# Performance work log

Hardware: AMD Instinct MI355X
Metric: run time of the kernel (lower is better)

The kernel has to match this reference:

```python
import jax, jax.numpy as jnp
import numpy as np

N_SRC0, N_DST0, FAN0 = 768000, 51200, 15
N_DST1, FAN1 = 5120, 10
N_DST2, FAN2 = 1024, 5
D_IN, D_HID, N_CLS = 128, 256, 47


def setup_inputs() -> dict:
    key = jax.random.key(0)
    ks = jax.random.split(key, 14)
    feats = jax.random.normal(ks[0], (N_SRC0, D_IN), jnp.float32)
    idx0 = jax.random.randint(ks[1], (N_DST0, FAN0), 0, N_SRC0)
    idx1 = jax.random.randint(ks[2], (N_DST1, FAN1), 0, N_DST0)
    idx2 = jax.random.randint(ks[3], (N_DST2, FAN2), 0, N_DST1)
    inverse_idx = jax.random.permutation(ks[4], N_DST0)
    s0 = 1.0 / np.sqrt(D_IN)
    s1 = 1.0 / np.sqrt(D_HID)
    return {
        "feats": feats,
        "W_self0": jax.random.normal(ks[5], (D_IN, D_HID), jnp.float32) * s0,
        "W_neigh0": jax.random.normal(ks[6], (D_IN, D_HID), jnp.float32) * s0,
        "b0": jnp.zeros((D_HID,), jnp.float32),
        "W_self1": jax.random.normal(ks[7], (D_HID, D_HID), jnp.float32) * s1,
        "W_neigh1": jax.random.normal(ks[8], (D_HID, D_HID), jnp.float32) * s1,
        "b1": jnp.zeros((D_HID,), jnp.float32),
        "W_self2": jax.random.normal(ks[9], (D_HID, N_CLS), jnp.float32) * s1,
        "W_neigh2": jax.random.normal(ks[10], (D_HID, N_CLS), jnp.float32) * s1,
        "b2": jnp.zeros((N_CLS,), jnp.float32),
        "idx0": idx0,
        "idx1": idx1,
        "idx2": idx2,
        "inverse_idx": inverse_idx,
    }


def _sage_mean(h, idx, W_self, W_neigh, b):
    # DGL SAGEConv('mean'): out = h_dst @ W_self + mean_neighbors(h) @ W_neigh + b
    h_dst = h[: idx.shape[0]]              # dst nodes are the first src nodes
    h_nb = jnp.take(h, idx, axis=0)        # [n_dst, fan, d] neighbor gather
    h_nb = h_nb.mean(axis=1)               # mean aggregation
    return h_dst @ W_self + h_nb @ W_neigh + b


def reference(feats, W_self0, W_neigh0, b0, W_self1, W_neigh1, b1,
              W_self2, W_neigh2, b2, idx0, idx1, idx2, inverse_idx):
    h = _sage_mean(feats, idx0, W_self0, W_neigh0, b0)
    h = h[inverse_idx]                     # NPFeatureShuffle inverse permutation
    h = jax.nn.relu(h)                     # dropout p=0 (eval)
    h = _sage_mean(h, idx1, W_self1, W_neigh1, b1)
    h = jax.nn.relu(h)
    h = _sage_mean(h, idx2, W_self2, W_neigh2, b2)
    return h
```

## Files before the change

kernel.cpp:

```cpp
#include <hip/hip_runtime.h>
#include <hip/hip_bf16.h>

#define N_SRC0 768000
#define N_DST0 51200
#define FAN0 15
#define N_DST1 5120
#define FAN1 10
#define N_DST2 1024
#define FAN2 5
#define D_IN 128
#define D_HID 256
#define N_CLS 47

#define TILES0 3200
#define GRID0 512

typedef __attribute__((ext_vector_type(4))) float f32x4;
typedef __attribute__((ext_vector_type(8))) short bf16x8;

static __device__ __forceinline__ unsigned pack_bf16(float x, float y) {
    __hip_bfloat16 hx = __float2bfloat16(x);
    __hip_bfloat16 hy = __float2bfloat16(y);
    unsigned short ux = *(unsigned short*)&hx;
    unsigned short uy = *(unsigned short*)&hy;
    return (unsigned)ux | ((unsigned)uy << 16);
}

__global__ void prep_weights(const float* __restrict__ Ws0, const float* __restrict__ Wn0,
                             const float* __restrict__ Ws1, const float* __restrict__ Wn1,
                             const float* __restrict__ Ws2, const float* __restrict__ Wn2,
                             float* __restrict__ Wc2,
                             __hip_bfloat16* __restrict__ Wt0b,
                             __hip_bfloat16* __restrict__ Wt1b)
{
    int t = blockIdx.x * blockDim.x + threadIdx.x;
    const int n2 = D_HID * N_CLS;
    if (t < n2) { Wc2[t] = Ws2[t]; Wc2[n2 + t] = Wn2[t]; }
    if (t < 65536) {
        int n = t >> 8, k = t & 255;
        float v = (k < 128) ? Ws0[k * 256 + n] : Wn0[(k - 128) * 256 + n];
        Wt0b[t] = __float2bfloat16(v);
    }
    if (t < 131072) {
        int n = t >> 9, k = t & 511;
        float v = (k < 256) ? Ws1[k * 256 + n] : Wn1[(k - 256) * 256 + n];
        Wt1b[t] = __float2bfloat16(v);
    }
}

__global__ __launch_bounds__(256, 2) void sage0_persist(
    const float* __restrict__ feats, const int* __restrict__ idx0,
    const int* __restrict__ inv, const __hip_bfloat16* __restrict__ Wt,
    const float* __restrict__ bias, unsigned short* __restrict__ H1b)
{
    __shared__ __align__(16) char xs[2][16 * 512];
    __shared__ int sidx[2][256];

    int tid = threadIdx.x;
    int bid = blockIdx.x;
    int w = tid >> 6, l = tid & 63;
    int lq = l & 15, kq = l >> 4;
    int rh = l >> 5, q = l & 31;

    bf16x8 B[4][8];
#pragma unroll
    for (int nt = 0; nt < 4; ++nt)
#pragma unroll
        for (int ks = 0; ks < 8; ++ks)
            B[nt][ks] = *(const bf16x8*)(Wt +
                (size_t)(w * 64 + nt * 16 + lq) * 256 + ks * 32 + kq * 8);
    float bv[4];
#pragma unroll
    for (int nt = 0; nt < 4; ++nt) bv[nt] = bias[w * 64 + nt * 16 + lq];

    int nIter = (TILES0 - bid + GRID0 - 1) / GRID0;

    {
        int r = tid >> 4, j = tid & 15;
        int rv = inv[bid * 16 + r];
        sidx[0][tid] = (j < 15) ? idx0[(size_t)rv * 15 + j] : rv;
    }
    __syncthreads();

    int pb = 0;
    for (int i = -1; i < nIter; ++i) {
        int t_cur = bid + i * GRID0;
        int t_nxt = t_cur + GRID0;
        bool mv = (i >= 0);
        bool gvv = (t_nxt < TILES0);
        int xb = pb ^ 1;
        const int* sp = sidx[pb];

        f32x4 acc[4];
#pragma unroll
        for (int nt = 0; nt < 4; ++nt) acc[nt] = (f32x4){0.f, 0.f, 0.f, 0.f};

        f32x4 s0 = (f32x4){0.f, 0.f, 0.f, 0.f};
#pragma unroll
        for (int ph = 0; ph < 4; ++ph) {
            int h = ph >> 1, jh = ph & 1;
            int r = w * 4 + h * 2 + rh;
            f32x4 g[8];
            if (gvv) {
                const int* sj = sp + r * 16 + jh * 8;
#pragma unroll
                for (int jj = 0; jj < 8; ++jj)
                    g[jj] = *(const f32x4*)&feats[(size_t)sj[jj] * 128 + q * 4];
            }
            if (mv) {
#pragma unroll
                for (int kss = 0; kss < 2; ++kss) {
                    int ks = ph * 2 + kss;
                    bf16x8 af = *(bf16x8*)(xs[pb] +
                        ((lq * 512 + ks * 64 + kq * 16) ^ ((lq & 7) << 4)));
#pragma unroll
                    for (int nt = 0; nt < 4; ++nt)
                        acc[nt] = __builtin_amdgcn_mfma_f32_16x16x32_bf16(
                            af, B[nt][ks], acc[nt], 0, 0, 0);
                }
            }
            if (gvv) {
                if (jh == 0) {
                    s0 = ((g[0] + g[1]) + (g[2] + g[3])) + ((g[4] + g[5]) + (g[6] + g[7]));
                } else {
                    f32x4 m = s0 + ((g[0] + g[1]) + (g[2] + g[3])) + ((g[4] + g[5]) + g[6]);
                    m *= (1.0f / 15.0f);
                    f32x4 sv = g[7];
                    uint2 ps = {pack_bf16(sv.x, sv.y), pack_bf16(sv.z, sv.w)};
                    uint2 pm = {pack_bf16(m.x, m.y), pack_bf16(m.z, m.w)};
                    int xorv = (r & 7) << 4;
                    *(uint2*)(xs[xb] + ((r * 512 + q * 8) ^ xorv)) = ps;
                    *(uint2*)(xs[xb] + ((r * 512 + 256 + q * 8) ^ xorv)) = pm;
                }
            }
        }

        if (mv) {
#pragma unroll
            for (int nt = 0; nt < 4; ++nt) {
#pragma unroll
                for (int qd = 0; qd < 4; ++qd) {
                    int row = t_cur * 16 + kq * 4 + qd;
                    float v = fmaxf(acc[nt][qd] + bv[nt], 0.f);
                    __hip_bfloat16 hb = __float2bfloat16(v);
                    H1b[(size_t)row * 256 + w * 64 + nt * 16 + lq] =
                        *(unsigned short*)&hb;
                }
            }
        }

        int t_n2 = t_nxt + GRID0;
        if (t_n2 < TILES0) {
            int r = tid >> 4, j = tid & 15;
            int rv = inv[t_n2 * 16 + r];
            sidx[xb][tid] = (j < 15) ? idx0[(size_t)rv * 15 + j] : rv;
        }
        __syncthreads();
        pb ^= 1;
    }
}

__global__ __launch_bounds__(512) void sage1_fused(
    const unsigned short* __restrict__ H1b, const int* __restrict__ idx1,
    const __hip_bfloat16* __restrict__ Wt,
    const float* __restrict__ bias, float* __restrict__ H2)
{
    __shared__ __align__(16) char xs[16 * 1024];
    __shared__ int sidx[16 * 12];

    int tid = threadIdx.x;
    int i0 = blockIdx.x * 16;

    for (int p = tid; p < 16 * 10; p += 512) {
        int r = p / 10, j = p % 10;
        sidx[r * 12 + j] = idx1[(size_t)(i0 + r) * 10 + j];
    }
    __syncthreads();

    int w = tid >> 6;
    int l = tid & 63;
    int rh = l >> 5, q = l & 31;

    {
        int r = w * 2 + rh;
        const int* sj = sidx + r * 12;
        uint4 sv = *(const uint4*)&H1b[(size_t)(i0 + r) * 256 + q * 8];
        f32x4 a0 = (f32x4){0.f, 0.f, 0.f, 0.f};
        f32x4 a1 = (f32x4){0.f, 0.f, 0.f, 0.f};
#pragma unroll
        for (int j = 0; j < 10; ++j) {
            uint4 nv = *(const uint4*)&H1b[(size_t)sj[j] * 256 + q * 8];
            a0.x += __uint_as_float(nv.x << 16);
            a0.y += __uint_as_float(nv.x & 0xffff0000u);
            a0.z += __uint_as_float(nv.y << 16);
            a0.w += __uint_as_float(nv.y & 0xffff0000u);
            a1.x += __uint_as_float(nv.z << 16);
            a1.y += __uint_as_float(nv.z & 0xffff0000u);
            a1.z += __uint_as_float(nv.w << 16);
            a1.w += __uint_as_float(nv.w & 0xffff0000u);
        }
        a0 *= (1.0f / 10.0f);
        a1 *= (1.0f / 10.0f);
        uint4 pm;
        pm.x = pack_bf16(a0.x, a0.y);
        pm.y = pack_bf16(a0.z, a0.w);
        pm.z = pack_bf16(a1.x, a1.y);
        pm.w = pack_bf16(a1.z, a1.w);
        int xorv = (r & 7) << 4;
        *(uint4*)(xs + ((r * 1024 + q * 16) ^ xorv)) = sv;
        *(uint4*)(xs + ((r * 1024 + 512 + q * 16) ^ xorv)) = pm;
    }
    __syncthreads();

    int arow = l & 15;
    int kq = l >> 4;
    int xorv_a = (arow & 7) << 4;

    f32x4 acc[2];
    acc[0] = (f32x4){0.f, 0.f, 0.f, 0.f};
    acc[1] = (f32x4){0.f, 0.f, 0.f, 0.f};

#pragma unroll
    for (int ks = 0; ks < 16; ++ks) {
        bf16x8 afrag = *(bf16x8*)(xs + ((arow * 1024 + ks * 64 + kq * 16) ^ xorv_a));
#pragma unroll
        for (int nt = 0; nt < 2; ++nt) {
            int n = w * 32 + nt * 16 + (l & 15);
            bf16x8 bfrag = *(const bf16x8*)(Wt + (size_t)n * 512 + ks * 32 + kq * 8);
            acc[nt] = __builtin_amdgcn_mfma_f32_16x16x32_bf16(afrag, bfrag, acc[nt], 0, 0, 0);
        }
    }

    int col0 = l & 15;
    int rq = l >> 4;
#pragma unroll
    for (int nt = 0; nt < 2; ++nt) {
        int col = w * 32 + nt * 16 + col0;
        float bvv = bias[col];
#pragma unroll
        for (int qd = 0; qd < 4; ++qd) {
            int row = i0 + rq * 4 + qd;
            H2[(size_t)row * 256 + col] = fmaxf(acc[nt][qd] + bvv, 0.f);
        }
    }
}

__global__ __launch_bounds__(256) void layer2(const float* __restrict__ H2,
                                              const int* __restrict__ idx2,
                                              const float* __restrict__ Wc2,
                                              const float* __restrict__ b2,
                                              float* __restrict__ out)
{
    __shared__ float xsf[512];
    __shared__ float part[4][64];
    int d = blockIdx.x;
    int t = threadIdx.x;
    const int* id = idx2 + (size_t)d * FAN2;

    xsf[t] = H2[(size_t)d * 256 + t];
    float a = 0.f;
#pragma unroll
    for (int j = 0; j < FAN2; ++j)
        a += H2[(size_t)id[j] * 256 + t];
    xsf[256 + t] = a * (1.0f / FAN2);
    __syncthreads();

    int c = t & 63;
    int kq = t >> 6;
    float s = 0.f;
    if (c < N_CLS) {
        int kbase = kq * 128;
#pragma unroll 8
        for (int k = 0; k < 128; ++k)
            s = fmaf(xsf[kbase + k], Wc2[(size_t)(kbase + k) * N_CLS + c], s);
    }
    part[kq][c] = s;
    __syncthreads();
    if (t < N_CLS) {
        float v = part[0][t] + part[1][t] + part[2][t] + part[3][t] + b2[t];
        out[(size_t)d * N_CLS + t] = v;
    }
}

extern "C" void kernel_launch(void* const* d_in, const int* in_sizes, int n_in,
                              void* d_out, int out_size, void* d_ws, size_t ws_size,
                              hipStream_t stream)
{
    const float* feats = (const float*)d_in[0];
    const float* Ws0 = (const float*)d_in[1];
    const float* Wn0 = (const float*)d_in[2];
    const float* b0  = (const float*)d_in[3];
    const float* Ws1 = (const float*)d_in[4];
    const float* Wn1 = (const float*)d_in[5];
    const float* b1  = (const float*)d_in[6];
    const float* Ws2 = (const float*)d_in[7];
    const float* Wn2 = (const float*)d_in[8];
    const float* b2  = (const float*)d_in[9];
    const int* idx0 = (const int*)d_in[10];
    const int* idx1 = (const int*)d_in[11];
    const int* idx2 = (const int*)d_in[12];
    const int* inv  = (const int*)d_in[13];

    char* ws = (char*)d_ws;
    unsigned short* H1b = (unsigned short*)ws;
    float* H2  = (float*)(ws + (size_t)N_DST0 * 256 * 2);
    float* Wc2 = H2 + (size_t)N_DST1 * 256;
    __hip_bfloat16* Wt0b = (__hip_bfloat16*)(Wc2 + 2 * D_HID * N_CLS);
    __hip_bfloat16* Wt1b = Wt0b + 256 * 256;

    prep_weights<<<dim3(512), dim3(256), 0, stream>>>(Ws0, Wn0, Ws1, Wn1, Ws2, Wn2,
                                                      Wc2, Wt0b, Wt1b);
    sage0_persist<<<dim3(GRID0), dim3(256), 0, stream>>>(feats, idx0, inv, Wt0b,
                                                         b0, H1b);
    sage1_fused<<<dim3(N_DST1 / 16), dim3(512), 0, stream>>>(H1b, idx1, Wt1b, b1, H2);
    layer2<<<dim3(N_DST2), dim3(256), 0, stream>>>(H2, idx2, Wc2, b2, (float*)d_out);
}
```

Measured before the change: 110.3 us.

## Fold weight prep into layer kernels and process two rows per layer2 block

Removes the separate prep_weights launch. sage0_persist now converts W0 to bf16 directly from the fp32 source while loading its register tiles, and its 512 blocks also write the transposed bf16 W1 for the next kernel. layer2 reads Ws2/Wn2 directly instead of a concatenated copy and handles two destination rows per block so each weight load is reused twice. This saves one launch and some global traffic, but the per-element strided fp32 loads of W0 in every block may make the kernel prologue more expensive.

After: 134.8 us. +22.2%, slower.

```diff
diff --git a/kernel.cpp b/kernel.cpp
--- a/kernel.cpp
+++ b/kernel.cpp
@@ -26,32 +26,18 @@
     return (unsigned)ux | ((unsigned)uy << 16);
 }
 
-__global__ void prep_weights(const float* __restrict__ Ws0, const float* __restrict__ Wn0,
-                             const float* __restrict__ Ws1, const float* __restrict__ Wn1,
-                             const float* __restrict__ Ws2, const float* __restrict__ Wn2,
-                             float* __restrict__ Wc2,
-                             __hip_bfloat16* __restrict__ Wt0b,
-                             __hip_bfloat16* __restrict__ Wt1b)
-{
-    int t = blockIdx.x * blockDim.x + threadIdx.x;
-    const int n2 = D_HID * N_CLS;
-    if (t < n2) { Wc2[t] = Ws2[t]; Wc2[n2 + t] = Wn2[t]; }
-    if (t < 65536) {
-        int n = t >> 8, k = t & 255;
-        float v = (k < 128) ? Ws0[k * 256 + n] : Wn0[(k - 128) * 256 + n];
-        Wt0b[t] = __float2bfloat16(v);
-    }
-    if (t < 131072) {
-        int n = t >> 9, k = t & 511;
-        float v = (k < 256) ? Ws1[k * 256 + n] : Wn1[(k - 256) * 256 + n];
-        Wt1b[t] = __float2bfloat16(v);
-    }
+static __device__ __forceinline__ short f2bf_s(float v) {
+    __hip_bfloat16 hb = __float2bfloat16(v);
+    return *(short*)&hb;
 }
 
 __global__ __launch_bounds__(256, 2) void sage0_persist(
     const float* __restrict__ feats, const int* __restrict__ idx0,
-    const int* __restrict__ inv, const __hip_bfloat16* __restrict__ Wt,
-    const float* __restrict__ bias, unsigned short* __restrict__ H1b)
+    const int* __restrict__ inv,
+    const float* __restrict__ Ws0, const float* __restrict__ Wn0,
+    const float* __restrict__ Ws1, const float* __restrict__ Wn1,
+    const float* __restrict__ bias, unsigned short* __restrict__ H1b,
+    __hip_bfloat16* __restrict__ Wt1b)
 {
     __shared__ __align__(16) char xs[2][16 * 512];
     __shared__ int sidx[2][256];
@@ -62,24 +48,42 @@
     int lq = l & 15, kq = l >> 4;
     int rh = l >> 5, q = l & 31;
 
-    bf16x8 B[4][8];
-#pragma unroll
-    for (int nt = 0; nt < 4; ++nt)
-#pragma unroll
-        for (int ks = 0; ks < 8; ++ks)
-            B[nt][ks] = *(const bf16x8*)(Wt +
-                (size_t)(w * 64 + nt * 16 + lq) * 256 + ks * 32 + kq * 8);
-    float bv[4];
-#pragma unroll
-    for (int nt = 0; nt < 4; ++nt) bv[nt] = bias[w * 64 + nt * 16 + lq];
-
-    int nIter = (TILES0 - bid + GRID0 - 1) / GRID0;
-
     {
         int r = tid >> 4, j = tid & 15;
         int rv = inv[bid * 16 + r];
         sidx[0][tid] = (j < 15) ? idx0[(size_t)rv * 15 + j] : rv;
     }
+
+    {
+        int t = bid * 256 + tid;
+        int n = t >> 9, k = t & 511;
+        float v = (k < 256) ? Ws1[k * 256 + n] : Wn1[(k - 256) * 256 + n];
+        Wt1b[t] = __float2bfloat16(v);
+    }
+
+    bf16x8 B[4][8];
+#pragma unroll
+    for (int nt = 0; nt < 4; ++nt) {
+#pragma unroll
+        for (int ks = 0; ks < 8; ++ks) {
+            int n = w * 64 + nt * 16 + lq;
+            int k0 = ks * 32 + kq * 8;
+            bf16x8 bv;
+#pragma unroll
+            for (int e = 0; e < 8; ++e) {
+                int k = k0 + e;
+                float v = (k < 128) ? Ws0[k * 256 + n] : Wn0[(k - 128) * 256 + n];
+                bv[e] = f2bf_s(v);
+            }
+            B[nt][ks] = bv;
+        }
+    }
+    float bv[4];
+#pragma unroll
+    for (int nt = 0; nt < 4; ++nt) bv[nt] = bias[w * 64 + nt * 16 + lq];
+
+    int nIter = (TILES0 - bid + GRID0 - 1) / GRID0;
+
     __syncthreads();
 
     int pb = 0;
@@ -247,38 +251,55 @@
 
 __global__ __launch_bounds__(256) void layer2(const float* __restrict__ H2,
                                               const int* __restrict__ idx2,
-                                              const float* __restrict__ Wc2,
+                                              const float* __restrict__ Ws2,
+                                              const float* __restrict__ Wn2,
                                               const float* __restrict__ b2,
                                               float* __restrict__ out)
 {
-    __shared__ float xsf[512];
-    __shared__ float part[4][64];
-    int d = blockIdx.x;
+    __shared__ float xsf[512][2];
+    __shared__ float part[4][2][64];
+    int d0 = blockIdx.x * 2;
     int t = threadIdx.x;
-    const int* id = idx2 + (size_t)d * FAN2;
-
-    xsf[t] = H2[(size_t)d * 256 + t];
-    float a = 0.f;
-#pragma unroll
-    for (int j = 0; j < FAN2; ++j)
-        a += H2[(size_t)id[j] * 256 + t];
-    xsf[256 + t] = a * (1.0f / FAN2);
+
+#pragma unroll
+    for (int rr = 0; rr < 2; ++rr) {
+        int d = d0 + rr;
+        const int* id = idx2 + (size_t)d * FAN2;
+        float self = H2[(size_t)d * 256 + t];
+        float a = 0.f;
+#pragma unroll
+        for (int j = 0; j < FAN2; ++j)
+            a += H2[(size_t)id[j] * 256 + t];
+        xsf[t][rr] = self;
+        xsf[256 + t][rr] = a * (1.0f / FAN2);
+    }
     __syncthreads();
 
     int c = t & 63;
     int kq = t >> 6;
-    float s = 0.f;
+    float s0 = 0.f, s1 = 0.f;
     if (c < N_CLS) {
+        const float* Wp = (kq < 2) ? Ws2 : Wn2;
+        int kb = (kq < 2) ? kq * 128 : kq * 128 - 256;
         int kbase = kq * 128;
 #pragma unroll 8
-        for (int k = 0; k < 128; ++k)
-            s = fmaf(xsf[kbase + k], Wc2[(size_t)(kbase + k) * N_CLS + c], s);
-    }
-    part[kq][c] = s;
-    __syncthreads();
-    if (t < N_CLS) {
-        float v = part[0][t] + part[1][t] + part[2][t] + part[3][t] + b2[t];
-        out[(size_t)d * N_CLS + t] = v;
+        for (int k = 0; k < 128; ++k) {
+            float wv = Wp[(size_t)(kb + k) * N_CLS + c];
+            float2 xv = *(const float2*)&xsf[kbase + k][0];
+            s0 = fmaf(xv.x, wv, s0);
+            s1 = fmaf(xv.y, wv, s1);
+        }
+    }
+    part[kq][0][c] = s0;
+    part[kq][1][c] = s1;
+    __syncthreads();
+    if (t < 128) {
+        int rr = t >> 6, cc = t & 63;
+        if (cc < N_CLS) {
+            float v = part[0][rr][cc] + part[1][rr][cc] + part[2][rr][cc]
+                    + part[3][rr][cc] + b2[cc];
+            out[(size_t)(d0 + rr) * N_CLS + cc] = v;
+        }
     }
 }
 
@@ -304,14 +325,12 @@
     char* ws = (char*)d_ws;
     unsigned short* H1b = (unsigned short*)ws;
     float* H2  = (float*)(ws + (size_t)N_DST0 * 256 * 2);
-    float* Wc2 = H2 + (size_t)N_DST1 * 256;
-    __hip_bfloat16* Wt0b = (__hip_bfloat16*)(Wc2 + 2 * D_HID * N_CLS);
-    __hip_bfloat16* Wt1b = Wt0b + 256 * 256;
-
-    prep_weights<<<dim3(512), dim3(256), 0, stream>>>(Ws0, Wn0, Ws1, Wn1, Ws2, Wn2,
-                                                      Wc2, Wt0b, Wt1b);
-    sage0_persist<<<dim3(GRID0), dim3(256), 0, stream>>>(feats, idx0, inv, Wt0b,
-                                                         b0, H1b);
+    __hip_bfloat16* Wt1b = (__hip_bfloat16*)(H2 + (size_t)N_DST1 * 256);
+
+    sage0_persist<<<dim3(GRID0), dim3(256), 0, stream>>>(feats, idx0, inv,
+                                                         Ws0, Wn0, Ws1, Wn1,
+                                                         b0, H1b, Wt1b);
     sage1_fused<<<dim3(N_DST1 / 16), dim3(512), 0, stream>>>(H1b, idx1, Wt1b, b1, H2);
-    layer2<<<dim3(N_DST2), dim3(256), 0, stream>>>(H2, idx2, Wc2, b2, (float*)d_out);
-}
+    layer2<<<dim3(N_DST2 / 2), dim3(256), 0, stream>>>(H2, idx2, Ws2, Wn2, b2,
+                                                       (float*)d_out);
+}
```

## Use atomic work-stealing tile scheduler in layer0 and two rows per block in layer2

Applied to the files above, without the earlier changes.

The persistent layer-0 kernel now takes tiles from a global atomic counter, which prep_weights resets, instead of a static round-robin stride. This is meant to balance load across blocks whose gather latency varies. The two-stage prefetch pipeline is kept by tracking the current, gathering and filling tiles through shared slots. Separately, the final layer kernel processes two destination rows per block so each Wc2 load feeds two FMAs, halving weight traffic and the block count, at the cost of an atomic per tile and a little extra shared-memory bookkeeping.

New measurement: 117.2 us. +6.2%, slower.

```diff
diff --git a/kernel.cpp b/kernel.cpp
--- a/kernel.cpp
+++ b/kernel.cpp
@@ -31,9 +31,11 @@
                              const float* __restrict__ Ws2, const float* __restrict__ Wn2,
                              float* __restrict__ Wc2,
                              __hip_bfloat16* __restrict__ Wt0b,
-                             __hip_bfloat16* __restrict__ Wt1b)
+                             __hip_bfloat16* __restrict__ Wt1b,
+                             int* __restrict__ ctr)
 {
     int t = blockIdx.x * blockDim.x + threadIdx.x;
+    if (t == 0) *ctr = GRID0;
     const int n2 = D_HID * N_CLS;
     if (t < n2) { Wc2[t] = Ws2[t]; Wc2[n2 + t] = Wn2[t]; }
     if (t < 65536) {
@@ -51,10 +53,12 @@
 __global__ __launch_bounds__(256, 2) void sage0_persist(
     const float* __restrict__ feats, const int* __restrict__ idx0,
     const int* __restrict__ inv, const __hip_bfloat16* __restrict__ Wt,
-    const float* __restrict__ bias, unsigned short* __restrict__ H1b)
+    const float* __restrict__ bias, unsigned short* __restrict__ H1b,
+    int* __restrict__ ctr)
 {
     __shared__ __align__(16) char xs[2][16 * 512];
     __shared__ int sidx[2][256];
+    __shared__ int snext[2];
 
     int tid = threadIdx.x;
     int bid = blockIdx.x;
@@ -73,21 +77,21 @@
 #pragma unroll
     for (int nt = 0; nt < 4; ++nt) bv[nt] = bias[w * 64 + nt * 16 + lq];
 
-    int nIter = (TILES0 - bid + GRID0 - 1) / GRID0;
-
     {
         int r = tid >> 4, j = tid & 15;
         int rv = inv[bid * 16 + r];
         sidx[0][tid] = (j < 15) ? idx0[(size_t)rv * 15 + j] : rv;
     }
-    __syncthreads();
-
+    if (tid == 0) snext[0] = atomicAdd(ctr, 1);
+    __syncthreads();
+
+    int t_cur = -1;
+    int t_gat = bid;
     int pb = 0;
-    for (int i = -1; i < nIter; ++i) {
-        int t_cur = bid + i * GRID0;
-        int t_nxt = t_cur + GRID0;
-        bool mv = (i >= 0);
-        bool gvv = (t_nxt < TILES0);
+    for (;;) {
+        bool mv = (t_cur >= 0 && t_cur < TILES0);
+        bool gvv = (t_gat < TILES0);
+        if (!mv && !gvv) break;
         int xb = pb ^ 1;
         const int* sp = sidx[pb];
 
@@ -149,13 +153,16 @@
             }
         }
 
-        int t_n2 = t_nxt + GRID0;
-        if (t_n2 < TILES0) {
+        int t_fill = snext[pb];
+        if (tid == 0) snext[xb] = atomicAdd(ctr, 1);
+        if (t_fill < TILES0) {
             int r = tid >> 4, j = tid & 15;
-            int rv = inv[t_n2 * 16 + r];
+            int rv = inv[t_fill * 16 + r];
             sidx[xb][tid] = (j < 15) ? idx0[(size_t)rv * 15 + j] : rv;
         }
         __syncthreads();
+        t_cur = t_gat;
+        t_gat = t_fill;
         pb ^= 1;
     }
 }
@@ -251,34 +258,48 @@
                                               const float* __restrict__ b2,
                                               float* __restrict__ out)
 {
-    __shared__ float xsf[512];
-    __shared__ float part[4][64];
-    int d = blockIdx.x;
+    __shared__ float xsf[512][2];
+    __shared__ float part[4][2][64];
+    int d0 = blockIdx.x * 2;
     int t = threadIdx.x;
-    const int* id = idx2 + (size_t)d * FAN2;
-
-    xsf[t] = H2[(size_t)d * 256 + t];
-    float a = 0.f;
-#pragma unroll
-    for (int j = 0; j < FAN2; ++j)
-        a += H2[(size_t)id[j] * 256 + t];
-    xsf[256 + t] = a * (1.0f / FAN2);
+
+#pragma unroll
+    for (int rr = 0; rr < 2; ++rr) {
+        int d = d0 + rr;
+        const int* id = idx2 + (size_t)d * FAN2;
+        float self = H2[(size_t)d * 256 + t];
+        float a = 0.f;
+#pragma unroll
+        for (int j = 0; j < FAN2; ++j)
+            a += H2[(size_t)id[j] * 256 + t];
+        xsf[t][rr] = self;
+        xsf[256 + t][rr] = a * (1.0f / FAN2);
+    }
     __syncthreads();
 
     int c = t & 63;
     int kq = t >> 6;
-    float s = 0.f;
+    float s0 = 0.f, s1 = 0.f;
     if (c < N_CLS) {
         int kbase = kq * 128;
 #pragma unroll 8
-        for (int k = 0; k < 128; ++k)
-            s = fmaf(xsf[kbase + k], Wc2[(size_t)(kbase + k) * N_CLS + c], s);
-    }
-    part[kq][c] = s;
-    __syncthreads();
-    if (t < N_CLS) {
-        float v = part[0][t] + part[1][t] + part[2][t] + part[3][t] + b2[t];
-        out[(size_t)d * N_CLS + t] = v;
+        for (int k = 0; k < 128; ++k) {
+            float wv = Wc2[(size_t)(kbase + k) * N_CLS + c];
+            float2 xv = *(const float2*)&xsf[kbase + k][0];
+            s0 = fmaf(xv.x, wv, s0);
+            s1 = fmaf(xv.y, wv, s1);
+        }
+    }
+    part[kq][0][c] = s0;
+    part[kq][1][c] = s1;
+    __syncthreads();
+    if (t < 128) {
+        int rr = t >> 6, cc = t & 63;
+        if (cc < N_CLS) {
+            float v = part[0][rr][cc] + part[1][rr][cc] + part[2][rr][cc]
+                    + part[3][rr][cc] + b2[cc];
+            out[(size_t)(d0 + rr) * N_CLS + cc] = v;
+        }
     }
 }
 
@@ -307,11 +328,13 @@
     float* Wc2 = H2 + (size_t)N_DST1 * 256;
     __hip_bfloat16* Wt0b = (__hip_bfloat16*)(Wc2 + 2 * D_HID * N_CLS);
     __hip_bfloat16* Wt1b = Wt0b + 256 * 256;
+    int* ctr = (int*)(Wt1b + 256 * 512);
 
     prep_weights<<<dim3(512), dim3(256), 0, stream>>>(Ws0, Wn0, Ws1, Wn1, Ws2, Wn2,
-                                                      Wc2, Wt0b, Wt1b);
+                                                      Wc2, Wt0b, Wt1b, ctr);
     sage0_persist<<<dim3(GRID0), dim3(256), 0, stream>>>(feats, idx0, inv, Wt0b,
-                                                         b0, H1b);
+                                                         b0, H1b, ctr);
     sage1_fused<<<dim3(N_DST1 / 16), dim3(512), 0, stream>>>(H1b, idx1, Wt1b, b1, H2);
-    layer2<<<dim3(N_DST2), dim3(256), 0, stream>>>(H2, idx2, Wc2, b2, (float*)d_out);
-}
+    layer2<<<dim3(N_DST2 / 2), dim3(256), 0, stream>>>(H2, idx2, Wc2, b2,
+                                                       (float*)d_out);
+}
```
